# Kernel tuning notes

Hardware: AMD Instinct MI355X
Metric: run time of the kernel (lower is better)

Reference implementation:

```python
import jax, jax.numpy as jnp
import numpy as np
from jax import lax

B, T, H = 64, 1024, 512
K = 10            # gaussian mixtures
U, V = 64, 80     # char steps, alphabet size
S = 3             # stroke dims


def setup_inputs() -> dict:
    key = jax.random.key(0)
    k1, k2, k3, k4 = jax.random.split(key, 4)
    return {
        "input0": jax.random.normal(k1, (B, T, H), dtype=jnp.float32),
        "stroke": jax.random.normal(k2, (B, T, S), dtype=jnp.float32),
        "char": jax.random.uniform(k3, (B, U, V), dtype=jnp.float32),
        "window_w": jax.random.normal(k4, (H, 3 * K), dtype=jnp.float32) * 0.05,
        "window_b": jnp.zeros((3 * K,), dtype=jnp.float32),
        "kappa0": jnp.zeros((B, K, 1), dtype=jnp.float32),
    }


def reference(input0, stroke, char, window_w, window_b, kappa0):
    u = jnp.arange(char.shape[1], dtype=input0.dtype)  # [U]
    k_mix = kappa0.shape[1]

    def step(kappa_prev, xs):
        x_t, s_t = xs  # [B,H], [B,S]
        abk = jnp.exp(x_t @ window_w + window_b)          # [B,3K]
        abk = abk.reshape(-1, 3 * k_mix, 1)               # [B,3K,1]
        alpha, beta, kappa_hat = jnp.split(abk, 3, axis=1)  # each [B,K,1]
        kappa = kappa_hat + kappa_prev                    # cumulative kappa state
        # phi_k = alpha * exp(-beta * (kappa - u)^2) -> sum over mixtures
        phi = jnp.sum(alpha * jnp.exp(-beta * jnp.square(kappa - u)), axis=1)  # [B,U]
        window = jnp.einsum('bu,buv->bv', phi, char)      # [B,V]
        out = jnp.concatenate((x_t, window, s_t), axis=1)  # [B,H+V+S]
        return kappa, out

    xs = (jnp.swapaxes(input0, 0, 1), jnp.swapaxes(stroke, 0, 1))  # [T,B,*]
    _, outs = lax.scan(step, kappa0, xs)
    return jnp.swapaxes(outs, 0, 1)  # [B,T,H+V+S]
```

## Files before the change

### kernel.cpp

```cpp
#include <hip/hip_runtime.h>

#define BB 64
#define TT 1024
#define BT (BB * TT)
#define HH 512
#define KMIX 10
#define UU 64
#define VV 80
#define SDIM 3
#define OUTW 595
#define ROWS 16

__global__ __launch_bounds__(256) void kW_transpose(const float* __restrict__ Wm, float* __restrict__ Wt) {
    int idx = blockIdx.x * 256 + threadIdx.x;
    if (idx < 30 * HH) {
        int j = idx >> 9, h = idx & 511;
        Wt[idx] = Wm[h * 30 + j];
    }
}

__global__ __launch_bounds__(512) void k1_gemm(
    const float* __restrict__ x,
    const float* __restrict__ stroke,
    const float* __restrict__ Wt,
    const float* __restrict__ bias,
    float* __restrict__ out,
    float* __restrict__ abk_t)
{
    __shared__ float xs[ROWS][HH + 4];
    const int tid = threadIdx.x;
    const int r0 = blockIdx.x * ROWS;

    const float4* x4 = (const float4*)(x + (size_t)r0 * HH);
    #pragma unroll
    for (int i = 0; i < 4; ++i) {
        int f4 = tid + (i << 9);
        int row = f4 >> 7;
        int col = (f4 & 127) << 2;
        float4 v = x4[f4];
        *(float4*)&xs[row][col] = v;
        float* orow = out + (size_t)(r0 + row) * OUTW + col;
        orow[0] = v.x; orow[1] = v.y; orow[2] = v.z; orow[3] = v.w;
    }
    if (tid < ROWS * SDIM) {
        int row = tid / SDIM, c = tid % SDIM;
        out[(size_t)(r0 + row) * OUTW + HH + VV + c] = stroke[(size_t)(r0 + row) * SDIM + c];
    }
    __syncthreads();

    const bool active = tid < 480;
    float acc[ROWS];
    if (active) {
        int hc = tid / 30, j = tid % 30;
        const float4* wp = (const float4*)(Wt + j * HH + hc * 32);
        float4 w4[8];
        #pragma unroll
        for (int q = 0; q < 8; ++q) w4[q] = wp[q];
        #pragma unroll
        for (int r = 0; r < ROWS; ++r) {
            const float4* xp = (const float4*)&xs[r][(tid / 30) * 32];
            float s = 0.f;
            #pragma unroll
            for (int q = 0; q < 8; ++q) {
                float4 xv = xp[q];
                s += xv.x * w4[q].x + xv.y * w4[q].y + xv.z * w4[q].z + xv.w * w4[q].w;
            }
            acc[r] = s;
        }
    }
    __syncthreads();
    float* plds = &xs[0][0];
    if (active) {
        #pragma unroll
        for (int r = 0; r < ROWS; ++r) plds[r * 480 + tid] = acc[r];
    }
    __syncthreads();
    if (active) {
        int row = tid & 15, jj = tid >> 4;
        float s = 0.f;
        #pragma unroll
        for (int q = 0; q < 16; ++q) s += plds[row * 480 + q * 30 + jj];
        abk_t[(size_t)jj * BT + r0 + row] = expf(s + bias[jj]);
    }
}

__global__ __launch_bounds__(64) void k2_scan(
    float* __restrict__ abk_t, const float* __restrict__ kappa0)
{
    const int b = blockIdx.x / KMIX;
    const int k = blockIdx.x % KMIX;
    const int lane = threadIdx.x;
    float4* p4 = (float4*)(abk_t + (size_t)(20 + k) * BT + b * TT);

    float v[16];
    #pragma unroll
    for (int i = 0; i < 4; ++i) {
        float4 q = p4[lane * 4 + i];
        v[i * 4 + 0] = q.x; v[i * 4 + 1] = q.y; v[i * 4 + 2] = q.z; v[i * 4 + 3] = q.w;
    }
    #pragma unroll
    for (int i = 1; i < 16; ++i) v[i] += v[i - 1];

    float total = v[15], xinc = total;
    #pragma unroll
    for (int off = 1; off < 64; off <<= 1) {
        float y = __shfl_up(xinc, off, 64);
        if (lane >= off) xinc += y;
    }
    float excl = xinc - total + kappa0[b * KMIX + k];

    #pragma unroll
    for (int i = 0; i < 4; ++i) {
        float4 q;
        q.x = v[i * 4 + 0] + excl; q.y = v[i * 4 + 1] + excl;
        q.z = v[i * 4 + 2] + excl; q.w = v[i * 4 + 3] + excl;
        p4[lane * 4 + i] = q;
    }
}

__global__ __launch_bounds__(256) void k3_window(
    const float* __restrict__ abk_t,
    const float* __restrict__ ch,
    float* __restrict__ out)
{
    __shared__ float cst[VV][68];
    __shared__ float win[4][UU * 81];
    const int b = blockIdx.x >> 2;
    const int qtr = blockIdx.x & 3;
    const int tid = threadIdx.x;
    const int wave = tid >> 6, lane = tid & 63;

    const float4* c4 = (const float4*)(ch + (size_t)b * UU * VV);
    #pragma unroll
    for (int i = 0; i < 5; ++i) {
        int f4 = tid + i * 256;
        float4 v = c4[f4];
        int f = f4 * 4;
        int u = f / 80;
        int v0 = f - u * 80;
        cst[v0][u] = v.x; cst[v0 + 1][u] = v.y; cst[v0 + 2][u] = v.z; cst[v0 + 3][u] = v.w;
    }
    __syncthreads();

    const int rb = b * TT + qtr * 256 + wave * 64;

    float ab[30];
    #pragma unroll
    for (int j = 0; j < 30; ++j) ab[j] = abk_t[(size_t)j * BT + rb + lane];

    float phi[UU];
    #pragma unroll
    for (int u = 0; u < UU; ++u) {
        float s = 0.f;
        const float uf = (float)u;
        #pragma unroll
        for (int k = 0; k < KMIX; ++k) {
            float d = ab[20 + k] - uf;
            s += ab[k] * __expf(-ab[10 + k] * d * d);
        }
        phi[u] = s;
    }

    float* winw = win[wave];
    for (int v = 0; v < VV; ++v) {
        float a = 0.f;
        #pragma unroll
        for (int q = 0; q < 16; ++q) {
            float4 cq = *(const float4*)&cst[v][q * 4];
            a += phi[q * 4 + 0] * cq.x + phi[q * 4 + 1] * cq.y
               + phi[q * 4 + 2] * cq.z + phi[q * 4 + 3] * cq.w;
        }
        winw[lane * 81 + v] = a;
    }

    for (int i = lane; i < UU * VV; i += 64) {
        int t = i / 80, v = i - t * 80;
        out[(size_t)(rb + t) * OUTW + HH + v] = winw[t * 81 + v];
    }
}

extern "C" void kernel_launch(void* const* d_in, const int* in_sizes, int n_in,
                              void* d_out, int out_size, void* d_ws, size_t ws_size,
                              hipStream_t stream) {
    const float* input0   = (const float*)d_in[0];
    const float* stroke   = (const float*)d_in[1];
    const float* chars    = (const float*)d_in[2];
    const float* window_w = (const float*)d_in[3];
    const float* window_b = (const float*)d_in[4];
    const float* kappa0   = (const float*)d_in[5];
    float* out   = (float*)d_out;
    float* abk_t = (float*)d_ws;
    float* Wt    = (float*)((char*)d_ws + (size_t)30 * BT * 4);

    kW_transpose<<<dim3((30 * HH + 255) / 256), dim3(256), 0, stream>>>(window_w, Wt);
    k1_gemm<<<dim3(BT / ROWS), dim3(512), 0, stream>>>(input0, stroke, Wt, window_b, out, abk_t);
    k2_scan<<<dim3(BB * KMIX), dim3(64), 0, stream>>>(abk_t, kappa0);
    k3_window<<<dim3(BB * 4), dim3(256), 0, stream>>>(abk_t, chars, out);
}
```

Before: 363.6 us.

## Fuse kappa scan into window kernel and rework GEMM to 256 threads

Removes the separate scan kernel: each window block recomputes the cumulative kappa prefix for its batch in shared memory, so the scanned kappa is never written back to global memory. The GEMM kernel drops to 256 threads, with each thread computing two output columns, and the input copy to the output becomes a row-contiguous coalesced store from LDS instead of strided scalar writes. The trade-offs are that each batch's scan is redone by four blocks, the window kernel uses more shared memory, and fewer GEMM threads are active.

```diff
diff --git a/kernel.cpp b/kernel.cpp
--- a/kernel.cpp
+++ b/kernel.cpp
@@ -19,7 +19,7 @@
     }
 }
 
-__global__ __launch_bounds__(512) void k1_gemm(
+__global__ __launch_bounds__(256) void k1_gemm(
     const float* __restrict__ x,
     const float* __restrict__ stroke,
     const float* __restrict__ Wt,
@@ -33,14 +33,9 @@
 
     const float4* x4 = (const float4*)(x + (size_t)r0 * HH);
     #pragma unroll
-    for (int i = 0; i < 4; ++i) {
-        int f4 = tid + (i << 9);
-        int row = f4 >> 7;
-        int col = (f4 & 127) << 2;
-        float4 v = x4[f4];
-        *(float4*)&xs[row][col] = v;
-        float* orow = out + (size_t)(r0 + row) * OUTW + col;
-        orow[0] = v.x; orow[1] = v.y; orow[2] = v.z; orow[3] = v.w;
+    for (int i = 0; i < 8; ++i) {
+        int f4 = tid + (i << 8);
+        *(float4*)&xs[f4 >> 7][(f4 & 127) << 2] = x4[f4];
     }
     if (tid < ROWS * SDIM) {
         int row = tid / SDIM, c = tid % SDIM;
@@ -48,87 +43,88 @@
     }
     __syncthreads();
 
-    const bool active = tid < 480;
-    float acc[ROWS];
+    #pragma unroll
+    for (int i = 0; i < 32; ++i) {
+        int idx = tid + (i << 8);
+        out[(size_t)(r0 + (idx >> 9)) * OUTW + (idx & 511)] = xs[idx >> 9][idx & 511];
+    }
+
+    const bool active = tid < 240;
+    float acc0[ROWS], acc1[ROWS];
     if (active) {
-        int hc = tid / 30, j = tid % 30;
-        const float4* wp = (const float4*)(Wt + j * HH + hc * 32);
-        float4 w4[8];
+        int hc = tid / 15, jp = tid % 15;
+        const float4* wp0 = (const float4*)(Wt + (2 * jp) * HH + hc * 32);
+        const float4* wp1 = (const float4*)(Wt + (2 * jp + 1) * HH + hc * 32);
+        float4 w0[8], w1[8];
         #pragma unroll
-        for (int q = 0; q < 8; ++q) w4[q] = wp[q];
+        for (int q = 0; q < 8; ++q) { w0[q] = wp0[q]; w1[q] = wp1[q]; }
         #pragma unroll
         for (int r = 0; r < ROWS; ++r) {
-            const float4* xp = (const float4*)&xs[r][(tid / 30) * 32];
-            float s = 0.f;
+            const float4* xp = (const float4*)&xs[r][(tid / 15) * 32];
+            float s0 = 0.f, s1 = 0.f;
             #pragma unroll
             for (int q = 0; q < 8; ++q) {
                 float4 xv = xp[q];
-                s += xv.x * w4[q].x + xv.y * w4[q].y + xv.z * w4[q].z + xv.w * w4[q].w;
+                s0 += xv.x * w0[q].x + xv.y * w0[q].y + xv.z * w0[q].z + xv.w * w0[q].w;
+                s1 += xv.x * w1[q].x + xv.y * w1[q].y + xv.z * w1[q].z + xv.w * w1[q].w;
             }
-            acc[r] = s;
+            acc0[r] = s0; acc1[r] = s1;
         }
     }
     __syncthreads();
     float* plds = &xs[0][0];
     if (active) {
+        int hc = tid / 15, jp = tid % 15;
         #pragma unroll
-        for (int r = 0; r < ROWS; ++r) plds[r * 480 + tid] = acc[r];
+        for (int r = 0; r < ROWS; ++r) {
+            *(float2*)&plds[hc * 480 + r * 30 + 2 * jp] = make_float2(acc0[r], acc1[r]);
+        }
     }
     __syncthreads();
-    if (active) {
-        int row = tid & 15, jj = tid >> 4;
+    for (int e = tid; e < 480; e += 256) {
+        int row = e & 15, jj = e >> 4;
         float s = 0.f;
         #pragma unroll
-        for (int q = 0; q < 16; ++q) s += plds[row * 480 + q * 30 + jj];
+        for (int q = 0; q < 16; ++q) s += plds[q * 480 + row * 30 + jj];
         abk_t[(size_t)jj * BT + r0 + row] = expf(s + bias[jj]);
     }
 }
 
-__global__ __launch_bounds__(64) void k2_scan(
-    float* __restrict__ abk_t, const float* __restrict__ kappa0)
-{
-    const int b = blockIdx.x / KMIX;
-    const int k = blockIdx.x % KMIX;
-    const int lane = threadIdx.x;
-    float4* p4 = (float4*)(abk_t + (size_t)(20 + k) * BT + b * TT);
-
-    float v[16];
-    #pragma unroll
-    for (int i = 0; i < 4; ++i) {
-        float4 q = p4[lane * 4 + i];
-        v[i * 4 + 0] = q.x; v[i * 4 + 1] = q.y; v[i * 4 + 2] = q.z; v[i * 4 + 3] = q.w;
-    }
-    #pragma unroll
-    for (int i = 1; i < 16; ++i) v[i] += v[i - 1];
-
-    float total = v[15], xinc = total;
-    #pragma unroll
-    for (int off = 1; off < 64; off <<= 1) {
-        float y = __shfl_up(xinc, off, 64);
-        if (lane >= off) xinc += y;
-    }
-    float excl = xinc - total + kappa0[b * KMIX + k];
-
-    #pragma unroll
-    for (int i = 0; i < 4; ++i) {
-        float4 q;
-        q.x = v[i * 4 + 0] + excl; q.y = v[i * 4 + 1] + excl;
-        q.z = v[i * 4 + 2] + excl; q.w = v[i * 4 + 3] + excl;
-        p4[lane * 4 + i] = q;
-    }
-}
-
-__global__ __launch_bounds__(256) void k3_window(
+__global__ __launch_bounds__(256) void k23_window(
     const float* __restrict__ abk_t,
+    const float* __restrict__ kappa0,
     const float* __restrict__ ch,
     float* __restrict__ out)
 {
+    __shared__ float kap[KMIX][TT];
     __shared__ float cst[VV][68];
     __shared__ float win[4][UU * 81];
     const int b = blockIdx.x >> 2;
     const int qtr = blockIdx.x & 3;
     const int tid = threadIdx.x;
     const int wave = tid >> 6, lane = tid & 63;
+
+    for (int k = wave; k < KMIX; k += 4) {
+        const float4* p4 = (const float4*)(abk_t + (size_t)(20 + k) * BT + b * TT);
+        float v[16];
+        #pragma unroll
+        for (int i = 0; i < 4; ++i) {
+            float4 q = p4[lane * 4 + i];
+            v[i * 4] = q.x; v[i * 4 + 1] = q.y; v[i * 4 + 2] = q.z; v[i * 4 + 3] = q.w;
+        }
+        #pragma unroll
+        for (int i = 1; i < 16; ++i) v[i] += v[i - 1];
+        float total = v[15], xinc = total;
+        #pragma unroll
+        for (int off = 1; off < 64; off <<= 1) {
+            float y = __shfl_up(xinc, off, 64);
+            if (lane >= off) xinc += y;
+        }
+        float excl = xinc - total + kappa0[b * KMIX + k];
+        float* kr = &kap[k][lane * 16];
+        #pragma unroll
+        for (int i = 0; i < 16; ++i) kr[i] = v[i] + excl;
+    }
 
     const float4* c4 = (const float4*)(ch + (size_t)b * UU * VV);
     #pragma unroll
@@ -142,11 +138,15 @@
     }
     __syncthreads();
 
-    const int rb = b * TT + qtr * 256 + wave * 64;
+    const int tl = qtr * 256 + tid;
+    const int rbg = b * TT + tl;
 
-    float ab[30];
+    float ab[20];
     #pragma unroll
-    for (int j = 0; j < 30; ++j) ab[j] = abk_t[(size_t)j * BT + rb + lane];
+    for (int j = 0; j < 20; ++j) ab[j] = abk_t[(size_t)j * BT + rbg];
+    float kp[KMIX];
+    #pragma unroll
+    for (int k = 0; k < KMIX; ++k) kp[k] = kap[k][tl];
 
     float phi[UU];
     #pragma unroll
@@ -155,7 +155,7 @@
         const float uf = (float)u;
         #pragma unroll
         for (int k = 0; k < KMIX; ++k) {
-            float d = ab[20 + k] - uf;
+            float d = kp[k] - uf;
             s += ab[k] * __expf(-ab[10 + k] * d * d);
         }
         phi[u] = s;
@@ -167,12 +167,13 @@
         #pragma unroll
         for (int q = 0; q < 16; ++q) {
             float4 cq = *(const float4*)&cst[v][q * 4];
-            a += phi[q * 4 + 0] * cq.x + phi[q * 4 + 1] * cq.y
+            a += phi[q * 4] * cq.x + phi[q * 4 + 1] * cq.y
                + phi[q * 4 + 2] * cq.z + phi[q * 4 + 3] * cq.w;
         }
         winw[lane * 81 + v] = a;
     }
 
+    const int rb = b * TT + qtr * 256 + wave * 64;
     for (int i = lane; i < UU * VV; i += 64) {
         int t = i / 80, v = i - t * 80;
         out[(size_t)(rb + t) * OUTW + HH + v] = winw[t * 81 + v];
@@ -193,7 +194,6 @@
     float* Wt    = (float*)((char*)d_ws + (size_t)30 * BT * 4);
 
     kW_transpose<<<dim3((30 * HH + 255) / 256), dim3(256), 0, stream>>>(window_w, Wt);
-    k1_gemm<<<dim3(BT / ROWS), dim3(512), 0, stream>>>(input0, stroke, Wt, window_b, out, abk_t);
-    k2_scan<<<dim3(BB * KMIX), dim3(64), 0, stream>>>(abk_t, kappa0);
-    k3_window<<<dim3(BB * 4), dim3(256), 0, stream>>>(abk_t, chars, out);
+    k1_gemm<<<dim3(BT / ROWS), dim3(256), 0, stream>>>(input0, stroke, Wt, window_b, out, abk_t);
+    k23_window<<<dim3(BB * 4), dim3(256), 0, stream>>>(abk_t, kappa0, chars, out);
 }
```

After: 367.0 us. Within noise of the previous version (+0.9%).
